# Kernel tuning notes

Hardware: AMD Instinct MI355X
Metric: run time of the kernel (lower is better)

## Reference

```python
import jax, jax.numpy as jnp
import numpy as np

NEG_SLOPE = 0.2


def gat_layer(x, W, a_src, a_dst, bias, src, dst, n_nodes):
    # x: [N, Fin]; W: [Fin, Fout]; a_src/a_dst: [Fout]; src/dst: [E] (self-loops included)
    h = x @ W                                  # [N, Fout]
    alpha_src = h @ a_src                      # [N]
    alpha_dst = h @ a_dst                      # [N]
    e = jax.nn.leaky_relu(alpha_src[src] + alpha_dst[dst], NEG_SLOPE)  # [E]
    # segment softmax over edges grouped by destination node
    m = jax.ops.segment_max(e, dst, num_segments=n_nodes)
    ex = jnp.exp(e - m[dst])
    s = jax.ops.segment_sum(ex, dst, num_segments=n_nodes)
    alpha = ex / s[dst]                        # every node has a self-loop -> s > 0
    out = jax.ops.segment_sum(alpha[:, None] * h[src], dst, num_segments=n_nodes)
    return out + bias


def setup_inputs() -> dict:
    key = jax.random.key(0)
    ks = jax.random.split(key, 16)
    N, E, F_IN = 100000, 1600000, 784
    d1, d2, d3 = 128, 256, 2
    x = jax.random.normal(ks[0], (N, F_IN), dtype=jnp.float32)
    edge_index = jax.random.randint(ks[1], (2, E), 0, N, dtype=jnp.int64)
    batch = jnp.zeros((N,), dtype=jnp.int64)

    def glorot(k, shape):
        fan_in, fan_out = shape[0], shape[-1]
        lim = float(np.sqrt(6.0 / (fan_in + fan_out)))
        return jax.random.uniform(k, shape, jnp.float32, -lim, lim)

    params = dict(
        W1=glorot(ks[2], (F_IN, d1)), a1s=glorot(ks[3], (d1,)), a1d=glorot(ks[4], (d1,)), b1=jnp.zeros((d1,), jnp.float32),
        W2=glorot(ks[5], (d1, d2)),  a2s=glorot(ks[6], (d2,)), a2d=glorot(ks[7], (d2,)), b2=jnp.zeros((d2,), jnp.float32),
        W3=glorot(ks[8], (d2, d3)),  a3s=glorot(ks[9], (d3,)), a3d=glorot(ks[10], (d3,)), b3=jnp.zeros((d3,), jnp.float32),
    )
    return dict(x=x, edge_index=edge_index, batch=batch, **params)


def reference(x, edge_index, batch,
              W1, a1s, a1d, b1,
              W2, a2s, a2d, b2,
              W3, a3s, a3d, b3):
    n_nodes = x.shape[0]
    # PyG GATConv default: add self-loops
    loop = jnp.arange(n_nodes, dtype=edge_index.dtype)
    src = jnp.concatenate([edge_index[0], loop])
    dst = jnp.concatenate([edge_index[1], loop])
    # dropout is identity in eval mode
    h = jax.nn.relu(gat_layer(x, W1, a1s, a1d, b1, src, dst, n_nodes))
    h = jax.nn.relu(gat_layer(h, W2, a2s, a2d, b2, src, dst, n_nodes))
    h = gat_layer(h, W3, a3s, a3d, b3, src, dst, n_nodes)
    return jax.nn.softmax(h, axis=1)
```

## Files before the change

### kernel.cpp

```cpp
#include <hip/hip_runtime.h>
#include <cstdint>

#define NEG_SLOPE 0.2f

typedef __attribute__((ext_vector_type(8))) short short8;
typedef __attribute__((ext_vector_type(4))) float f32x4;
typedef __attribute__((ext_vector_type(2))) float f32x2;
typedef __attribute__((ext_vector_type(4))) unsigned short ushort4v;
typedef __attribute__((ext_vector_type(2))) unsigned short ushort2v;

__device__ inline void split_bf16(float v, short& hi, short& lo) {
  unsigned u = __builtin_bit_cast(unsigned, v);
  hi = (short)(u >> 16);
  float hif = __builtin_bit_cast(float, u & 0xffff0000u);
  float r = v - hif;
  lo = (short)(__builtin_bit_cast(unsigned, r) >> 16);
}

__device__ inline float b2f(unsigned short u) {
  return __builtin_bit_cast(float, (unsigned)u << 16);
}
__device__ inline unsigned short f2b_rne(float f) {
  unsigned u = __builtin_bit_cast(unsigned, f);
  return (unsigned short)((u + 0x7fffu + ((u >> 16) & 1u)) >> 16);
}


__global__ __launch_bounds__(256) void hist_kernel(const int* __restrict__ ei,
                                                   int* __restrict__ deg, int E, int N) {
  int e = blockIdx.x * 256 + threadIdx.x;
  int total = E + N;
  if (e >= total) return;
  int d = (e < E) ? ei[E + e] : (e - E);
  atomicAdd(&deg[d], 1);
}


__global__ __launch_bounds__(256) void scan_phaseA(const int* __restrict__ deg,
                                                   int* __restrict__ bsum, int n) {
  __shared__ int red[256];
  int base = blockIdx.x * 1024;
  int s = 0;
#pragma unroll
  for (int j = 0; j < 4; j++) {
    int i = base + threadIdx.x + j * 256;
    if (i < n) s += deg[i];
  }
  red[threadIdx.x] = s;
  __syncthreads();
  for (int off = 128; off; off >>= 1) {
    if (threadIdx.x < off) red[threadIdx.x] += red[threadIdx.x + off];
    __syncthreads();
  }
  if (threadIdx.x == 0) bsum[blockIdx.x] = red[0];
}

__global__ __launch_bounds__(256) void scan_phaseB(int* __restrict__ bsum,
                                                   int* __restrict__ rowstart,
                                                   int nb, int n) {
  __shared__ int sc[256];
  int tid = threadIdx.x;
  int v = (tid < nb) ? bsum[tid] : 0;
  sc[tid] = v;
  __syncthreads();
  for (int off = 1; off < 256; off <<= 1) {
    int t = (tid >= off) ? sc[tid - off] : 0;
    __syncthreads();
    sc[tid] += t;
    __syncthreads();
  }
  if (tid < nb) bsum[tid] = sc[tid] - v;
  if (tid == 0) rowstart[n] = sc[255];
}

__global__ __launch_bounds__(256) void scan_phaseC(const int* __restrict__ deg,
                                                   const int* __restrict__ bsum,
                                                   int* __restrict__ rowstart,
                                                   int* __restrict__ cursor, int n) {
  __shared__ int tsum[256];
  int tid = threadIdx.x;
  int base = blockIdx.x * 1024 + tid * 4;
  int d[4];
  int s = 0;
#pragma unroll
  for (int j = 0; j < 4; j++) {
    int i = base + j;
    d[j] = (i < n) ? deg[i] : 0;
    s += d[j];
  }
  tsum[tid] = s;
  __syncthreads();
  for (int off = 1; off < 256; off <<= 1) {
    int t = (tid >= off) ? tsum[tid - off] : 0;
    __syncthreads();
    tsum[tid] += t;
    __syncthreads();
  }
  int run = bsum[blockIdx.x] + tsum[tid] - s;
#pragma unroll
  for (int j = 0; j < 4; j++) {
    int i = base + j;
    if (i < n) { rowstart[i] = run; cursor[i] = run; }
    run += d[j];
  }
}

__global__ __launch_bounds__(256) void scatter_kernel(const int* __restrict__ ei,
                                                      int* __restrict__ cursor,
                                                      int* __restrict__ csr_src, int E, int N) {
  int e = blockIdx.x * 256 + threadIdx.x;
  int total = E + N;
  if (e >= total) return;
  int s, d;
  if (e < E) { s = ei[e]; d = ei[E + e]; }
  else       { s = e - E; d = e - E; }
  int p = atomicAdd(&cursor[d], 1);
  csr_src[p] = s;
}


__global__ __launch_bounds__(256) void convw_kernel(const float* __restrict__ W,
                                                    short* __restrict__ Whi,
                                                    short* __restrict__ Wlo,
                                                    int K, int N, int Kp) {
  int idx = blockIdx.x * 256 + threadIdx.x;
  if (idx >= N * Kp) return;
  int n = idx / Kp, k = idx % Kp;
  float v = (k < K) ? W[(size_t)k * N + n] : 0.f;
  short hi, lo;
  split_bf16(v, hi, lo);
  Whi[idx] = hi;
  Wlo[idx] = lo;
}


#define LDK 40

__global__ __launch_bounds__(256, 2) void mfma_gemm_split(
    const float* __restrict__ A, const short* __restrict__ Bhi, const short* __restrict__ Blo,
    unsigned short* __restrict__ C, int M, int Nn, int K, int Kp) {
  __shared__ short Ah[128 * LDK], Al[128 * LDK], Bh[128 * LDK], Bl[128 * LDK];

  const int t = threadIdx.x;
  const int bm = blockIdx.x * 128;
  const int n0 = blockIdx.y * 128;

  const int srow = t >> 1;
  const int shalf = t & 1;
  const bool arow_ok = (bm + srow) < M;

  const int w = t >> 6, lane = t & 63;
  const int wm = (w >> 1) * 64, wn = (w & 1) * 64;
  const int lm = lane & 15, quad = lane >> 4;

  f32x4 acc[4][4];
#pragma unroll
  for (int i = 0; i < 4; i++)
#pragma unroll
    for (int j = 0; j < 4; j++) acc[i][j] = (f32x4)(0.f);

  for (int k0 = 0; k0 < Kp; k0 += 32) {
    __syncthreads();

    {
      const int kbase = k0 + shalf * 16;
      f32x4 v0 = (f32x4)(0.f), v1 = (f32x4)(0.f), v2 = (f32x4)(0.f), v3 = (f32x4)(0.f);
      if (arow_ok && kbase < K) {
        const f32x4* p = (const f32x4*)(A + (size_t)(bm + srow) * K + kbase);
        v0 = p[0]; v1 = p[1]; v2 = p[2]; v3 = p[3];
      }
      float f[16] = {v0[0], v0[1], v0[2], v0[3], v1[0], v1[1], v1[2], v1[3],
                     v2[0], v2[1], v2[2], v2[3], v3[0], v3[1], v3[2], v3[3]};
      short hi[16], lo[16];
#pragma unroll
      for (int j = 0; j < 16; j++) split_bf16(f[j], hi[j], lo[j]);
      const int la = srow * LDK + shalf * 16;
      *(short8*)&Ah[la] = *(short8*)&hi[0];
      *(short8*)&Ah[la + 8] = *(short8*)&hi[8];
      *(short8*)&Al[la] = *(short8*)&lo[0];
      *(short8*)&Al[la + 8] = *(short8*)&lo[8];
    }
    {
      const size_t gb = (size_t)(n0 + srow) * Kp + k0 + shalf * 16;
      const short8* ph = (const short8*)(Bhi + gb);
      const short8* pl = (const short8*)(Blo + gb);
      short8 h0 = ph[0], h1 = ph[1], l0 = pl[0], l1 = pl[1];
      const int la = srow * LDK + shalf * 16;
      *(short8*)&Bh[la] = h0;
      *(short8*)&Bh[la + 8] = h1;
      *(short8*)&Bl[la] = l0;
      *(short8*)&Bl[la + 8] = l1;
    }
    __syncthreads();

    short8 afh[4], afl[4], bfh[4], bfl[4];
#pragma unroll
    for (int i = 0; i < 4; i++) {
      const int ra = (wm + i * 16 + lm) * LDK + quad * 8;
      afh[i] = *(const short8*)&Ah[ra];
      afl[i] = *(const short8*)&Al[ra];
      const int rb = (wn + i * 16 + lm) * LDK + quad * 8;
      bfh[i] = *(const short8*)&Bh[rb];
      bfl[i] = *(const short8*)&Bl[rb];
    }
#pragma unroll
    for (int i = 0; i < 4; i++)
#pragma unroll
      for (int j = 0; j < 4; j++) {
        acc[i][j] = __builtin_amdgcn_mfma_f32_16x16x32_bf16(afh[i], bfh[j], acc[i][j], 0, 0, 0);
        acc[i][j] = __builtin_amdgcn_mfma_f32_16x16x32_bf16(afh[i], bfl[j], acc[i][j], 0, 0, 0);
        acc[i][j] = __builtin_amdgcn_mfma_f32_16x16x32_bf16(afl[i], bfh[j], acc[i][j], 0, 0, 0);
      }
  }

#pragma unroll
  for (int i = 0; i < 4; i++) {
    const int rbase = bm + wm + i * 16 + quad * 4;
#pragma unroll
    for (int j = 0; j < 4; j++) {
      const int c = n0 + wn + j * 16 + lm;
#pragma unroll
      for (int r = 0; r < 4; r++) {
        const int row = rbase + r;
        if (row < M) C[(size_t)row * Nn + c] = f2b_rne(acc[i][j][r]);
      }
    }
  }
}


__global__ __launch_bounds__(256) void alpha_kernel(const unsigned short* __restrict__ h,
                                                    const float* __restrict__ a_s,
                                                    const float* __restrict__ a_d,
                                                    float* __restrict__ as_,
                                                    float* __restrict__ ad_,
                                                    int N, int F) {
  int wid = (blockIdx.x * 256 + threadIdx.x) >> 6;
  int lane = threadIdx.x & 63;
  if (wid >= N) return;
  float ss = 0.f, dd = 0.f;
  for (int c = lane; c < F; c += 64) {
    float v = b2f(h[(int64_t)wid * F + c]);
    ss += v * a_s[c];
    dd += v * a_d[c];
  }
#pragma unroll
  for (int off = 32; off; off >>= 1) {
    ss += __shfl_down(ss, off);
    dd += __shfl_down(dd, off);
  }
  if (lane == 0) { as_[wid] = ss; ad_[wid] = dd; }
}


template <int VPL>
__global__ __launch_bounds__(256) void agg_kernel(const unsigned short* __restrict__ h,
                                                  const float* __restrict__ as_,
                                                  const float* __restrict__ ad_,
                                                  const int* __restrict__ rowstart,
                                                  const int* __restrict__ csr_src,
                                                  const float* __restrict__ bias,
                                                  float* __restrict__ out,
                                                  int N, int F, int do_relu) {
  int wid = (blockIdx.x * 256 + threadIdx.x) >> 6;
  int lane = threadIdx.x & 63;
  if (wid >= N) return;
  int r0 = rowstart[wid], r1 = rowstart[wid + 1];
  float adn = ad_[wid];

  float m = -1e30f;
  for (int i = r0 + lane; i < r1; i += 64) {
    float e = as_[csr_src[i]] + adn;
    e = e > 0.f ? e : NEG_SLOPE * e;
    m = fmaxf(m, e);
  }
#pragma unroll
  for (int off = 32; off; off >>= 1) m = fmaxf(m, __shfl_xor(m, off));

  float ssum = 0.f;
  for (int i = r0 + lane; i < r1; i += 64) {
    float e = as_[csr_src[i]] + adn;
    e = e > 0.f ? e : NEG_SLOPE * e;
    ssum += __expf(e - m);
  }
#pragma unroll
  for (int off = 32; off; off >>= 1) ssum += __shfl_xor(ssum, off);
  float inv = 1.f / ssum;

  const int cbase = lane * VPL;
  float acc[VPL];
#pragma unroll
  for (int v = 0; v < VPL; v++) acc[v] = 0.f;
  for (int k = r0; k < r1; k++) {
    int s = csr_src[k];
    float e = as_[s] + adn;
    e = e > 0.f ? e : NEG_SLOPE * e;
    float w = __expf(e - m);
    const unsigned short* hrow = h + (int64_t)s * F + cbase;
    unsigned short uv[VPL];
    if (VPL == 4) *(ushort4v*)uv = *(const ushort4v*)hrow;
    else          *(ushort2v*)uv = *(const ushort2v*)hrow;
#pragma unroll
    for (int v = 0; v < VPL; v++) acc[v] += w * b2f(uv[v]);
  }
  float ov[VPL];
#pragma unroll
  for (int v = 0; v < VPL; v++) {
    float o = acc[v] * inv + bias[cbase + v];
    if (do_relu) o = fmaxf(o, 0.f);
    ov[v] = o;
  }
  float* op = out + (int64_t)wid * F + cbase;
  if (VPL == 4) *(f32x4*)op = *(f32x4*)ov;
  else          *(f32x2*)op = *(f32x2*)ov;
}


__global__ __launch_bounds__(256) void gemm3_kernel(const float* __restrict__ h,
                                                    const float* __restrict__ W3,
                                                    const float* __restrict__ a3s,
                                                    const float* __restrict__ a3d,
                                                    float* __restrict__ h3,
                                                    float* __restrict__ as_,
                                                    float* __restrict__ ad_,
                                                    int N, int K) {
  int wid = (blockIdx.x * 256 + threadIdx.x) >> 6;
  int lane = threadIdx.x & 63;
  if (wid >= N) return;
  float c0 = 0.f, c1 = 0.f;
  for (int k = lane; k < K; k += 64) {
    float v = h[(int64_t)wid * K + k];
    c0 += v * W3[k * 2 + 0];
    c1 += v * W3[k * 2 + 1];
  }
#pragma unroll
  for (int off = 32; off; off >>= 1) {
    c0 += __shfl_down(c0, off);
    c1 += __shfl_down(c1, off);
  }
  if (lane == 0) {
    h3[wid * 2 + 0] = c0;
    h3[wid * 2 + 1] = c1;
    as_[wid] = c0 * a3s[0] + c1 * a3s[1];
    ad_[wid] = c0 * a3d[0] + c1 * a3d[1];
  }
}


__global__ __launch_bounds__(256) void agg3_kernel(const float* __restrict__ h3,
                                                   const float* __restrict__ as_,
                                                   const float* __restrict__ ad_,
                                                   const int* __restrict__ rowstart,
                                                   const int* __restrict__ csr_src,
                                                   const float* __restrict__ b3,
                                                   float* __restrict__ out, int N) {
  int wid = (blockIdx.x * 256 + threadIdx.x) >> 6;
  int lane = threadIdx.x & 63;
  if (wid >= N) return;
  int r0 = rowstart[wid], r1 = rowstart[wid + 1];
  float adn = ad_[wid];

  float m = -1e30f;
  for (int i = r0 + lane; i < r1; i += 64) {
    float e = as_[csr_src[i]] + adn;
    e = e > 0.f ? e : NEG_SLOPE * e;
    m = fmaxf(m, e);
  }
#pragma unroll
  for (int off = 32; off; off >>= 1) m = fmaxf(m, __shfl_xor(m, off));

  float ssum = 0.f, a0 = 0.f, a1 = 0.f;
  for (int i = r0 + lane; i < r1; i += 64) {
    int s = csr_src[i];
    float e = as_[s] + adn;
    e = e > 0.f ? e : NEG_SLOPE * e;
    float w = __expf(e - m);
    ssum += w;
    a0 += w * h3[s * 2 + 0];
    a1 += w * h3[s * 2 + 1];
  }
#pragma unroll
  for (int off = 32; off; off >>= 1) {
    ssum += __shfl_xor(ssum, off);
    a0 += __shfl_xor(a0, off);
    a1 += __shfl_xor(a1, off);
  }
  if (lane == 0) {
    float inv = 1.f / ssum;
    float o0 = a0 * inv + b3[0];
    float o1 = a1 * inv + b3[1];
    float mm = fmaxf(o0, o1);
    float e0 = __expf(o0 - mm), e1 = __expf(o1 - mm);
    float d = e0 + e1;
    out[wid * 2 + 0] = e0 / d;
    out[wid * 2 + 1] = e1 / d;
  }
}


extern "C" void kernel_launch(void* const* d_in, const int* in_sizes, int n_in,
                              void* d_out, int out_size, void* d_ws, size_t ws_size,
                              hipStream_t stream) {
  const float* x   = (const float*)d_in[0];
  const int*   ei  = (const int*)d_in[1];
  const float* W1  = (const float*)d_in[3];
  const float* a1s = (const float*)d_in[4];
  const float* a1d = (const float*)d_in[5];
  const float* b1  = (const float*)d_in[6];
  const float* W2  = (const float*)d_in[7];
  const float* a2s = (const float*)d_in[8];
  const float* a2d = (const float*)d_in[9];
  const float* b2  = (const float*)d_in[10];
  const float* W3  = (const float*)d_in[11];
  const float* a3s = (const float*)d_in[12];
  const float* a3d = (const float*)d_in[13];
  const float* b3  = (const float*)d_in[14];

  int N   = in_sizes[2];
  int E   = in_sizes[1] / 2;
  int FIN = in_sizes[0] / N;
  int d1  = in_sizes[4];
  int d2  = in_sizes[8];
  int Kp1 = ((FIN + 31) / 32) * 32;

  char* p = (char*)d_ws;
  unsigned short* hbuf = (unsigned short*)p; p += (size_t)N * d2 * sizeof(float);
  float* buf2 = (float*)p; p += (size_t)N * d2 * sizeof(float);
  float* h3   = (float*)p; p += (size_t)N * 2 * sizeof(float);
  float* as_  = (float*)p; p += (size_t)N * sizeof(float);
  float* ad_  = (float*)p; p += (size_t)N * sizeof(float);
  int* deg      = (int*)p; p += (size_t)N * sizeof(int);
  int* rowstart = (int*)p; p += (size_t)(N + 1) * sizeof(int);
  int* cursor   = (int*)p; p += (size_t)N * sizeof(int);
  int* bsum     = (int*)p; p += 1024 * sizeof(int);
  int* csr      = (int*)p; p += (size_t)(E + N) * sizeof(int);
  p = (char*)(((uintptr_t)p + 255) & ~(uintptr_t)255);
  short* w1h = (short*)p; p += (size_t)d1 * Kp1 * sizeof(short);
  short* w1l = (short*)p; p += (size_t)d1 * Kp1 * sizeof(short);
  short* w2h = (short*)p; p += (size_t)d2 * d1 * sizeof(short);
  short* w2l = (short*)p; p += (size_t)d2 * d1 * sizeof(short);

  hipMemsetAsync(deg, 0, (size_t)N * sizeof(int), stream);
  int tot = E + N;
  hist_kernel<<<(tot + 255) / 256, 256, 0, stream>>>(ei, deg, E, N);
  int nb = (N + 1023) / 1024;
  scan_phaseA<<<nb, 256, 0, stream>>>(deg, bsum, N);
  scan_phaseB<<<1, 256, 0, stream>>>(bsum, rowstart, nb, N);
  scan_phaseC<<<nb, 256, 0, stream>>>(deg, bsum, rowstart, cursor, N);
  scatter_kernel<<<(tot + 255) / 256, 256, 0, stream>>>(ei, cursor, csr, E, N);

  convw_kernel<<<(d1 * Kp1 + 255) / 256, 256, 0, stream>>>(W1, w1h, w1l, FIN, d1, Kp1);
  convw_kernel<<<(d2 * d1 + 255) / 256, 256, 0, stream>>>(W2, w2h, w2l, d1, d2, d1);

  int wb = (N + 3) / 4;

  {
    dim3 g((N + 127) / 128, d1 / 128);
    mfma_gemm_split<<<g, 256, 0, stream>>>(x, w1h, w1l, hbuf, N, d1, FIN, Kp1);
    alpha_kernel<<<wb, 256, 0, stream>>>(hbuf, a1s, a1d, as_, ad_, N, d1);
    agg_kernel<2><<<wb, 256, 0, stream>>>(hbuf, as_, ad_, rowstart, csr, b1, buf2, N, d1, 1);
  }
  {
    dim3 g((N + 127) / 128, d2 / 128);
    mfma_gemm_split<<<g, 256, 0, stream>>>(buf2, w2h, w2l, hbuf, N, d2, d1, d1);
    alpha_kernel<<<wb, 256, 0, stream>>>(hbuf, a2s, a2d, as_, ad_, N, d2);
    agg_kernel<4><<<wb, 256, 0, stream>>>(hbuf, as_, ad_, rowstart, csr, b2, buf2, N, d2, 1);
  }
  {
    gemm3_kernel<<<wb, 256, 0, stream>>>(buf2, W3, a3s, a3d, h3, as_, ad_, N, d2);
    agg3_kernel<<<wb, 256, 0, stream>>>(h3, as_, ad_, rowstart, csr, b3, (float*)d_out, N);
  }
}
```

Before: 1.259 ms.

## Use online softmax, unroll gather by four, vectorize alpha loads

The aggregation kernel now computes the segment max and exp-sum in a single online-softmax pass instead of two passes over the edge list. Its gather loop is unrolled by four so several independent row loads are in flight at once, which targets gather latency. The alpha kernel now reads four bf16 values per lane with a vector load. The trade-off is extra exp calls in the online softmax and higher register pressure from the unrolling.

```diff
diff --git a/kernel.cpp b/kernel.cpp
--- a/kernel.cpp
+++ b/kernel.cpp
@@ -24,6 +24,7 @@
   unsigned u = __builtin_bit_cast(unsigned, f);
   return (unsigned short)((u + 0x7fffu + ((u >> 16) & 1u)) >> 16);
 }
+__device__ inline float leaky(float e) { return e > 0.f ? e : NEG_SLOPE * e; }
 
 
 __global__ __launch_bounds__(256) void hist_kernel(const int* __restrict__ ei,
@@ -239,10 +240,14 @@
   int lane = threadIdx.x & 63;
   if (wid >= N) return;
   float ss = 0.f, dd = 0.f;
-  for (int c = lane; c < F; c += 64) {
-    float v = b2f(h[(int64_t)wid * F + c]);
-    ss += v * a_s[c];
-    dd += v * a_d[c];
+  for (int c = lane * 4; c < F; c += 256) {
+    ushort4v uv = *(const ushort4v*)(h + (int64_t)wid * F + c);
+#pragma unroll
+    for (int v = 0; v < 4; v++) {
+      float x = b2f(uv[v]);
+      ss += x * a_s[c + v];
+      dd += x * a_d[c + v];
+    }
   }
 #pragma unroll
   for (int off = 32; off; off >>= 1) {
@@ -268,34 +273,54 @@
   int r0 = rowstart[wid], r1 = rowstart[wid + 1];
   float adn = ad_[wid];
 
-  float m = -1e30f;
+  float m = -1e30f, ssum = 0.f;
   for (int i = r0 + lane; i < r1; i += 64) {
-    float e = as_[csr_src[i]] + adn;
-    e = e > 0.f ? e : NEG_SLOPE * e;
-    m = fmaxf(m, e);
-  }
-#pragma unroll
-  for (int off = 32; off; off >>= 1) m = fmaxf(m, __shfl_xor(m, off));
-
-  float ssum = 0.f;
-  for (int i = r0 + lane; i < r1; i += 64) {
-    float e = as_[csr_src[i]] + adn;
-    e = e > 0.f ? e : NEG_SLOPE * e;
-    ssum += __expf(e - m);
-  }
-#pragma unroll
-  for (int off = 32; off; off >>= 1) ssum += __shfl_xor(ssum, off);
+    float e = leaky(as_[csr_src[i]] + adn);
+    float mn = fmaxf(m, e);
+    ssum = ssum * __expf(m - mn) + __expf(e - mn);
+    m = mn;
+  }
+#pragma unroll
+  for (int off = 32; off; off >>= 1) {
+    float mo = __shfl_xor(m, off);
+    float so = __shfl_xor(ssum, off);
+    float mn = fmaxf(m, mo);
+    ssum = ssum * __expf(m - mn) + so * __expf(mo - mn);
+    m = mn;
+  }
   float inv = 1.f / ssum;
 
   const int cbase = lane * VPL;
   float acc[VPL];
 #pragma unroll
   for (int v = 0; v < VPL; v++) acc[v] = 0.f;
-  for (int k = r0; k < r1; k++) {
+
+  int k = r0;
+  for (; k + 4 <= r1; k += 4) {
+    int s0 = csr_src[k], s1 = csr_src[k + 1], s2 = csr_src[k + 2], s3 = csr_src[k + 3];
+    float w0 = __expf(leaky(as_[s0] + adn) - m);
+    float w1 = __expf(leaky(as_[s1] + adn) - m);
+    float w2 = __expf(leaky(as_[s2] + adn) - m);
+    float w3 = __expf(leaky(as_[s3] + adn) - m);
+    unsigned short u0[VPL], u1[VPL], u2[VPL], u3[VPL];
+    if (VPL == 4) {
+      *(ushort4v*)u0 = *(const ushort4v*)(h + (int64_t)s0 * F + cbase);
+      *(ushort4v*)u1 = *(const ushort4v*)(h + (int64_t)s1 * F + cbase);
+      *(ushort4v*)u2 = *(const ushort4v*)(h + (int64_t)s2 * F + cbase);
+      *(ushort4v*)u3 = *(const ushort4v*)(h + (int64_t)s3 * F + cbase);
+    } else {
+      *(ushort2v*)u0 = *(const ushort2v*)(h + (int64_t)s0 * F + cbase);
+      *(ushort2v*)u1 = *(const ushort2v*)(h + (int64_t)s1 * F + cbase);
+      *(ushort2v*)u2 = *(const ushort2v*)(h + (int64_t)s2 * F + cbase);
+      *(ushort2v*)u3 = *(const ushort2v*)(h + (int64_t)s3 * F + cbase);
+    }
+#pragma unroll
+    for (int v = 0; v < VPL; v++)
+      acc[v] += w0 * b2f(u0[v]) + w1 * b2f(u1[v]) + w2 * b2f(u2[v]) + w3 * b2f(u3[v]);
+  }
+  for (; k < r1; k++) {
     int s = csr_src[k];
-    float e = as_[s] + adn;
-    e = e > 0.f ? e : NEG_SLOPE * e;
-    float w = __expf(e - m);
+    float w = __expf(leaky(as_[s] + adn) - m);
     const unsigned short* hrow = h + (int64_t)s * F + cbase;
     unsigned short uv[VPL];
     if (VPL == 4) *(ushort4v*)uv = *(const ushort4v*)hrow;
@@ -303,6 +328,7 @@
 #pragma unroll
     for (int v = 0; v < VPL; v++) acc[v] += w * b2f(uv[v]);
   }
+
   float ov[VPL];
 #pragma unroll
   for (int v = 0; v < VPL; v++) {
@@ -362,8 +388,7 @@
 
   float m = -1e30f;
   for (int i = r0 + lane; i < r1; i += 64) {
-    float e = as_[csr_src[i]] + adn;
-    e = e > 0.f ? e : NEG_SLOPE * e;
+    float e = leaky(as_[csr_src[i]] + adn);
     m = fmaxf(m, e);
   }
 #pragma unroll
@@ -372,8 +397,7 @@
   float ssum = 0.f, a0 = 0.f, a1 = 0.f;
   for (int i = r0 + lane; i < r1; i += 64) {
     int s = csr_src[i];
-    float e = as_[s] + adn;
-    e = e > 0.f ? e : NEG_SLOPE * e;
+    float e = leaky(as_[s] + adn);
     float w = __expf(e - m);
     ssum += w;
     a0 += w * h3[s * 2 + 0];
```

Result: faster. 1.073 ms (-14.7%).
